# Performance work log

Hardware: AMD Instinct MI355X
Metric: run time of the kernel (lower is better)

## Reference

```python
import jax, jax.numpy as jnp
import numpy as np

B, T, D, H, E, M = 4, 2048, 2048, 8, 512, 8  # batch, seq, hidden, moe_heads, moe_experts, moe_dim//2
F = E * M  # flatten_shape = 4096
HALF = D // 2


def act(z):
    # 'relu2' activation: relu(x)**2
    r = jax.nn.relu(z)
    return r * r


def setup_inputs() -> dict:
    key = jax.random.key(0)
    ks = jax.random.split(key, 13)
    s = 0.02
    return {
        "x": jax.random.normal(ks[0], (B, T, D), jnp.float32),
        "g1": jax.random.uniform(ks[1], (B, T, H, E), jnp.float32),
        "g2": jax.random.uniform(ks[2], (B, T, H, E), jnp.float32),
        "u1_w": jax.random.normal(ks[3], (F, D), jnp.float32) * s,
        "u1_b": jnp.zeros((F,), jnp.float32),
        "u2_w": jax.random.normal(ks[4], (F, D), jnp.float32) * s,
        "u2_b": jnp.zeros((F,), jnp.float32),
        "v11_w": jax.random.normal(ks[5], (HALF, F), jnp.float32) * s,
        "v12_w": jax.random.normal(ks[6], (HALF, F), jnp.float32) * s,
        "v21_w": jax.random.normal(ks[7], (HALF, F), jnp.float32) * s,
        "v22_w": jax.random.normal(ks[8], (HALF, F), jnp.float32) * s,
        "b1": jax.random.normal(ks[9], (E, HALF), jnp.float32) * s,
        "b2": jax.random.normal(ks[10], (E, HALF), jnp.float32) * s,
    }


def reference(x, g1, g2, u1_w, u1_b, u2_w, u2_b, v11_w, v12_w, v21_w, v22_w, b1, b2):
    # x1, x2: [B,T,E,M]
    x1 = act(x @ u1_w.T + u1_b).reshape(B, T, E, M)
    x2 = act(x @ u2_w.T + u2_b).reshape(B, T, E, M)

    g1s = g1.sum(axis=2)  # [B,T,E] (einsum '...hi->...i')
    g2s = g2.sum(axis=2)

    # x11 = v11(einsum('btim,bthi->btim', x1, g1).flatten(-2))
    x11 = (x1 * g1s[..., None]).reshape(B, T, F) @ v11_w.T
    # x12 = v12(einsum('btjm,bthj,bthi->btim', x2, g2, g1).flatten(-2))
    t2 = jnp.einsum('btjm,bthj->bthm', x2, g2)
    x12 = jnp.einsum('bthm,bthi->btim', t2, g1).reshape(B, T, F) @ v12_w.T
    # x13 = einsum('bthi,id->btd', g1, b1)
    x13 = g1s @ b1

    # x21 = v21(einsum('btim,bthi,bthj->btjm', x1, g1, g2).flatten(-2))
    t1 = jnp.einsum('btim,bthi->bthm', x1, g1)
    x21 = jnp.einsum('bthm,bthj->btjm', t1, g2).reshape(B, T, F) @ v21_w.T
    # x22 = v22(einsum('btjm,bthj->btjm', x2, g2).flatten(-2))
    x22 = (x2 * g2s[..., None]).reshape(B, T, F) @ v22_w.T
    # x23 = einsum('bthj,jd->btd', g2, b2)
    x23 = g2s @ b2

    return jnp.concatenate((x11 + x12 + x13, x21 + x22 + x23), axis=-1)
```

## Files before the change

kernel.cpp:

```cpp
#include <hip/hip_runtime.h>
#include <hip/hip_bf16.h>

#define TOK   8192
#define DD    2048
#define FF    4096
#define EE    512
#define HALF  1024
#define KCAT  8704

typedef __bf16 bf16x8 __attribute__((ext_vector_type(8)));
typedef __bf16 bf16x4 __attribute__((ext_vector_type(4)));
typedef float  f32x4  __attribute__((ext_vector_type(4)));
using bf16 = __hip_bfloat16;

#define AS1(p) ((const __attribute__((address_space(1))) void*)(p))
#define AS3(p) ((__attribute__((address_space(3))) void*)(p))


__global__ void cvt_bf16(const float* __restrict__ in, bf16* __restrict__ out, int n4) {
    int i = blockIdx.x * blockDim.x + threadIdx.x;
    int stride = gridDim.x * blockDim.x;
    for (; i < n4; i += stride) {
        float4 v = ((const float4*)in)[i];
        bf16x4 o;
        o[0] = (__bf16)v.x; o[1] = (__bf16)v.y; o[2] = (__bf16)v.z; o[3] = (__bf16)v.w;
        ((bf16x4*)out)[i] = o;
    }
}

__global__ void pack_w(const float* __restrict__ vA, const float* __restrict__ vB,
                       const float* __restrict__ bmat, bf16* __restrict__ W) {
    int n = blockIdx.x;
    const float* ra = vA + (size_t)n * FF;
    const float* rb = vB + (size_t)n * FF;
    bf16* w = W + (size_t)n * KCAT;
    for (int k = threadIdx.x; k < FF; k += 256) {
        w[k]      = __float2bfloat16(ra[k]);
        w[FF + k] = __float2bfloat16(rb[k]);
    }
    for (int e = threadIdx.x; e < EE; e += 256)
        w[2 * FF + e] = __float2bfloat16(bmat[(size_t)e * HALF + n]);
}

template<int MODE>
__global__ __launch_bounds__(512, 2)
void gemmP(const bf16* __restrict__ A0, const bf16* __restrict__ B0,
           const float* __restrict__ bias0, void* __restrict__ C0,
           const bf16* __restrict__ A1, const bf16* __restrict__ B1,
           const float* __restrict__ bias1, void* __restrict__ C1,
           int nbm, int nbn, int K, int ldc)
{
    __shared__ __align__(16) char smem[131072];
    const int tid  = threadIdx.x;
    const int lane = tid & 63;
    const int wid  = tid >> 6;
    const int wm = wid >> 2, wn = wid & 3;
    const int r16 = lane & 15, kb = lane >> 4;

    int bid = blockIdx.x;
    {
        int nwg = gridDim.x;
        int q = nwg >> 3, r = nwg & 7;
        int xcd = bid & 7, idx = bid >> 3;
        bid = (xcd < r ? xcd * (q + 1) : r * (q + 1) + (xcd - r) * q) + idx;
    }
    const int npg = nbm * nbn;
    const int g   = bid / npg;
    const int lb  = bid - g * npg;
    const int bm = lb / nbn, bn = lb - bm * nbn;

    const bf16*  A    = g ? A1 : A0;
    const bf16*  Bw   = g ? B1 : B0;
    const float* bias = g ? bias1 : bias0;
    char* Cout = (char*)(g ? C1 : C0);

    const long row0 = (long)bm * 256;
    const int  col0 = bn * 256;
    const int  nt   = K >> 6;

    const char* gA[2]; const char* gB[2];
    #pragma unroll
    for (int l = 0; l < 2; ++l) {
        const uint32_t S = (uint32_t)(l * 512 + tid) * 16;
        const int r  = (int)(S >> 6);
        const int cb = (int)((S & 63) ^ ((uint32_t)((r >> 1) & 3) << 4));
        gA[l] = (const char*)A  + (row0 + r) * (long)K * 2 + cb;
        gB[l] = (const char*)Bw + (long)(col0 + r) * K * 2 + cb;
    }
    const uint32_t ldst = (uint32_t)(tid & ~63) * 16;

    const uint32_t swz  = ((uint32_t)(r16 >> 1) & 3u) << 4;
    const uint32_t aoff = (uint32_t)((wm * 128 + r16) * 64 + kb * 16) ^ swz;
    const uint32_t boff = (uint32_t)((wn * 64  + r16) * 64 + kb * 16) ^ swz;

    f32x4 acc[8][4];
    #pragma unroll
    for (int i = 0; i < 8; ++i)
        #pragma unroll
        for (int j = 0; j < 4; ++j)
            acc[i][j] = (f32x4){0.f, 0.f, 0.f, 0.f};

    __builtin_amdgcn_global_load_lds(AS1(gA[0]),      AS3(smem +     0 + ldst), 16, 0, 0);
    __builtin_amdgcn_global_load_lds(AS1(gA[1]),      AS3(smem +  8192 + ldst), 16, 0, 0);
    __builtin_amdgcn_global_load_lds(AS1(gB[0]),      AS3(smem + 32768 + ldst), 16, 0, 0);
    __builtin_amdgcn_global_load_lds(AS1(gB[1]),      AS3(smem + 40960 + ldst), 16, 0, 0);
    __builtin_amdgcn_global_load_lds(AS1(gA[0] + 64), AS3(smem + 16384 + ldst), 16, 0, 0);
    __builtin_amdgcn_global_load_lds(AS1(gA[1] + 64), AS3(smem + 24576 + ldst), 16, 0, 0);
    __builtin_amdgcn_global_load_lds(AS1(gB[0] + 64), AS3(smem + 49152 + ldst), 16, 0, 0);
    __builtin_amdgcn_global_load_lds(AS1(gB[1] + 64), AS3(smem + 57344 + ldst), 16, 0, 0);
    asm volatile("s_waitcnt vmcnt(4)\n\ts_barrier" ::: "memory");

    bf16x8 afA[4], afB[4], bv0[4], bv1[4];
    #pragma unroll
    for (int f = 0; f < 4; ++f) {
        afA[f] = *(const bf16x8*)(smem +     0 + aoff + f * 1024);
        bv0[f] = *(const bf16x8*)(smem + 32768 + boff + f * 1024);
    }

#define MFMA16(AF, BV, IH)                                                              \
    __builtin_amdgcn_s_setprio(1);                                                      \
    _Pragma("unroll")                                                                   \
    for (int fi = 0; fi < 4; ++fi) {                                                    \
        acc[(IH)*4+fi][0] = __builtin_amdgcn_mfma_f32_16x16x32_bf16(AF[fi], BV[0], acc[(IH)*4+fi][0], 0, 0, 0); \
        acc[(IH)*4+fi][1] = __builtin_amdgcn_mfma_f32_16x16x32_bf16(AF[fi], BV[1], acc[(IH)*4+fi][1], 0, 0, 0); \
        acc[(IH)*4+fi][2] = __builtin_amdgcn_mfma_f32_16x16x32_bf16(AF[fi], BV[2], acc[(IH)*4+fi][2], 0, 0, 0); \
        acc[(IH)*4+fi][3] = __builtin_amdgcn_mfma_f32_16x16x32_bf16(AF[fi], BV[3], acc[(IH)*4+fi][3], 0, 0, 0); \
    }                                                                                   \
    __builtin_amdgcn_s_setprio(0);

    for (int t = 0; t < nt; ++t) {
        const char* pb = smem + (t & 1) * 65536;
        char*       pt = smem + ((t + 1) & 1) * 65536;
        const bool  st = (t + 1 < nt);
        const long  koff = (long)(t + 1) * 128;

        if (st) {
            __builtin_amdgcn_global_load_lds(AS1(gA[0] + koff), AS3(pt +    0 + ldst), 16, 0, 0);
            __builtin_amdgcn_global_load_lds(AS1(gA[1] + koff), AS3(pt + 8192 + ldst), 16, 0, 0);
        }
        asm volatile("s_barrier" ::: "memory");
        #pragma unroll
        for (int f = 0; f < 4; ++f)
            afB[f] = *(const bf16x8*)(pb + 4096 + aoff + f * 1024);
        MFMA16(afA, bv0, 0)

        if (st) {
            __builtin_amdgcn_global_load_lds(AS1(gB[0] + koff), AS3(pt + 32768 + ldst), 16, 0, 0);
            __builtin_amdgcn_global_load_lds(AS1(gB[1] + koff), AS3(pt + 40960 + ldst), 16, 0, 0);
            asm volatile("s_waitcnt vmcnt(4)" ::: "memory");
        } else {
            asm volatile("s_waitcnt vmcnt(0)" ::: "memory");
        }
        asm volatile("s_barrier" ::: "memory");
        #pragma unroll
        for (int f = 0; f < 4; ++f) {
            afA[f] = *(const bf16x8*)(pb + 16384 + aoff + f * 1024);
            bv1[f] = *(const bf16x8*)(pb + 49152 + boff + f * 1024);
        }
        MFMA16(afB, bv0, 1)

        if (st) {
            __builtin_amdgcn_global_load_lds(AS1(gA[0] + koff + 64), AS3(pt + 16384 + ldst), 16, 0, 0);
            __builtin_amdgcn_global_load_lds(AS1(gA[1] + koff + 64), AS3(pt + 24576 + ldst), 16, 0, 0);
        }
        asm volatile("s_barrier" ::: "memory");
        #pragma unroll
        for (int f = 0; f < 4; ++f)
            afB[f] = *(const bf16x8*)(pb + 16384 + 4096 + aoff + f * 1024);
        MFMA16(afA, bv1, 0)

        if (st) {
            __builtin_amdgcn_global_load_lds(AS1(gB[0] + koff + 64), AS3(pt + 49152 + ldst), 16, 0, 0);
            __builtin_amdgcn_global_load_lds(AS1(gB[1] + koff + 64), AS3(pt + 57344 + ldst), 16, 0, 0);
            asm volatile("s_waitcnt vmcnt(4)" ::: "memory");
        }
        asm volatile("s_barrier" ::: "memory");
        if (st) {
            #pragma unroll
            for (int f = 0; f < 4; ++f) {
                afA[f] = *(const bf16x8*)(pt +     0 + aoff + f * 1024);
                bv0[f] = *(const bf16x8*)(pt + 32768 + boff + f * 1024);
            }
        }
        MFMA16(afB, bv1, 1)
    }
#undef MFMA16

    const int rb = (lane >> 4) * 4;
    #pragma unroll
    for (int i = 0; i < 8; ++i) {
        #pragma unroll
        for (int j = 0; j < 4; ++j) {
            const int cc = col0 + wn * 64 + j * 16 + r16;
            float badd = 0.f;
            if (MODE == 1) badd = bias[cc];
            #pragma unroll
            for (int e = 0; e < 4; ++e) {
                long row = row0 + wm * 128 + i * 16 + rb + e;
                float v = acc[i][j][e];
                if (MODE == 1) {
                    v += badd;
                    v = fmaxf(v, 0.f);
                    v = v * v;
                    ((bf16*)Cout)[row * ldc + cc] = __float2bfloat16(v);
                } else {
                    ((float*)Cout)[row * ldc + cc] = v;
                }
            }
        }
    }
}

#define GPAD 524
__global__ __launch_bounds__(256)
void glue(const float* __restrict__ g1, const float* __restrict__ g2,
          bf16* __restrict__ Yl, bf16* __restrict__ Yr)
{
    __shared__ __align__(16) float g1t[8 * GPAD];
    __shared__ __align__(16) float g2t[8 * GPAD];
    __shared__ float g1s[EE], g2s[EE];
    __shared__ float t1s[64], t2s[64];
    __shared__ float t1p[4][64], t2p[4][64];
    __shared__ __align__(16) bf16 x1t[FF], x2t[FF];

    const int t   = blockIdx.x;
    const int tid = threadIdx.x;
    const float* g1p = g1 + (size_t)t * FF;
    const float* g2p = g2 + (size_t)t * FF;
    bf16* ylp = Yl + (size_t)t * KCAT;
    bf16* yrp = Yr + (size_t)t * KCAT;

    #pragma unroll
    for (int c = 0; c < 4; ++c) {
        int idx4 = (c * 256 + tid) * 4;
        float4 v1 = *(const float4*)(g1p + idx4);
        float4 v2 = *(const float4*)(g2p + idx4);
        int h = idx4 >> 9, e = idx4 & 511;
        *(float4*)&g1t[h * GPAD + e] = v1;
        *(float4*)&g2t[h * GPAD + e] = v2;
    }
    #pragma unroll
    for (int c = 0; c < 2; ++c) {
        int idx8 = (c * 256 + tid) * 8;
        *(bf16x8*)&x1t[idx8] = *(const bf16x8*)(ylp + idx8);
        *(bf16x8*)&x2t[idx8] = *(const bf16x8*)(yrp + FF + idx8);
    }
    __syncthreads();

    #pragma unroll
    for (int c = 0; c < 2; ++c) {
        int e = c * 256 + tid;
        float s1 = 0.f, s2 = 0.f;
        #pragma unroll
        for (int h = 0; h < 8; ++h) { s1 += g1t[h * GPAD + e]; s2 += g2t[h * GPAD + e]; }
        g1s[e] = s1; g2s[e] = s2;
    }

    {
        int o = tid & 63;
        int h = o & 7, m = o >> 3;
        int p = tid >> 6;
        float s1 = 0.f, s2 = 0.f;
        #pragma unroll 8
        for (int ii = 0; ii < 128; ++ii) {
            int e = p * 128 + ii;
            float xv1 = __bfloat162float(x1t[e * 8 + m]);
            float xv2 = __bfloat162float(x2t[e * 8 + m]);
            s1 += xv1 * g1t[h * GPAD + e];
            s2 += xv2 * g2t[h * GPAD + e];
        }
        t1p[p][o] = s1; t2p[p][o] = s2;
    }
    __syncthreads();
    if (tid < 64)       t1s[tid] = t1p[0][tid] + t1p[1][tid] + t1p[2][tid] + t1p[3][tid];
    else if (tid < 128) { int o = tid - 64; t2s[o] = t2p[0][o] + t2p[1][o] + t2p[2][o] + t2p[3][o]; }
    __syncthreads();

    #pragma unroll
    for (int c = 0; c < 2; ++c) {
        int f0 = (c * 256 + tid) * 8;
        int e  = f0 >> 3;
        float s1 = g1s[e], s2 = g2s[e];
        bf16x8 xa = *(const bf16x8*)&x1t[f0];
        bf16x8 xb = *(const bf16x8*)&x2t[f0];
        bf16x8 o1, o2;
        #pragma unroll
        for (int u = 0; u < 8; ++u) {
            o1[u] = (__bf16)((float)xa[u] * s1);
            o2[u] = (__bf16)((float)xb[u] * s2);
        }
        *(bf16x8*)(ylp + f0)      = o1;
        *(bf16x8*)(yrp + FF + f0) = o2;
    }
    #pragma unroll
    for (int c = 0; c < 2; ++c) {
        int f0 = (c * 256 + tid) * 8;
        int i  = f0 >> 3;
        bf16x8 o12v, o21v;
        #pragma unroll
        for (int m = 0; m < 8; ++m) {
            float s12 = 0.f, s21 = 0.f;
            #pragma unroll
            for (int h = 0; h < 8; ++h) {
                s12 += t2s[(m << 3) | h] * g1t[h * GPAD + i];
                s21 += t1s[(m << 3) | h] * g2t[h * GPAD + i];
            }
            o12v[m] = (__bf16)s12;
            o21v[m] = (__bf16)s21;
        }
        *(bf16x8*)(ylp + FF + f0) = o12v;
        *(bf16x8*)(yrp + f0)      = o21v;
    }
    {
        int e0 = tid * 2;
        ylp[2 * FF + e0]     = __float2bfloat16(g1s[e0]);
        ylp[2 * FF + e0 + 1] = __float2bfloat16(g1s[e0 + 1]);
        yrp[2 * FF + e0]     = __float2bfloat16(g2s[e0]);
        yrp[2 * FF + e0 + 1] = __float2bfloat16(g2s[e0 + 1]);
    }
}


extern "C" void kernel_launch(void* const* d_in, const int* in_sizes, int n_in,
                              void* d_out, int out_size, void* d_ws, size_t ws_size,
                              hipStream_t stream) {
    const float* x    = (const float*)d_in[0];
    const float* g1   = (const float*)d_in[1];
    const float* g2   = (const float*)d_in[2];
    const float* u1_w = (const float*)d_in[3];
    const float* u1_b = (const float*)d_in[4];
    const float* u2_w = (const float*)d_in[5];
    const float* u2_b = (const float*)d_in[6];
    const float* v11  = (const float*)d_in[7];
    const float* v12  = (const float*)d_in[8];
    const float* v21  = (const float*)d_in[9];
    const float* v22  = (const float*)d_in[10];
    const float* b1   = (const float*)d_in[11];
    const float* b2   = (const float*)d_in[12];
    float* out = (float*)d_out;

    size_t off = 0;
    char* base = (char*)d_ws;
    auto take = [&](size_t bytes) { void* p = base + off; off += (bytes + 255) & ~(size_t)255; return p; };
    bf16* Xb  = (bf16*)take((size_t)TOK * DD * 2);
    bf16* U1b = (bf16*)take((size_t)FF * DD * 2);
    bf16* U2b = (bf16*)take((size_t)FF * DD * 2);
    bf16* Wl  = (bf16*)take((size_t)HALF * KCAT * 2);
    bf16* Wr  = (bf16*)take((size_t)HALF * KCAT * 2);
    bf16* Yl  = (bf16*)take((size_t)TOK * KCAT * 2);
    bf16* Yr  = (bf16*)take((size_t)TOK * KCAT * 2);

    cvt_bf16<<<4096, 256, 0, stream>>>(x,    Xb,  TOK * DD / 4);
    cvt_bf16<<<2048, 256, 0, stream>>>(u1_w, U1b, FF * DD / 4);
    cvt_bf16<<<2048, 256, 0, stream>>>(u2_w, U2b, FF * DD / 4);
    pack_w<<<HALF, 256, 0, stream>>>(v11, v12, b1, Wl);
    pack_w<<<HALF, 256, 0, stream>>>(v21, v22, b2, Wr);

    gemmP<1><<<2 * (TOK / 256) * (FF / 256), 512, 0, stream>>>(
        Xb, U1b, u1_b, Yl,
        Xb, U2b, u2_b, Yr + FF,
        TOK / 256, FF / 256, DD, KCAT);

    glue<<<TOK, 256, 0, stream>>>(g1, g2, Yl, Yr);

    gemmP<0><<<2 * (TOK / 256) * (HALF / 256), 512, 0, stream>>>(
        Yl, Wl, nullptr, out,
        Yr, Wr, nullptr, out + HALF,
        TOK / 256, HALF / 256, KCAT, DD);
}
```

Measured before the change: 692.9 us.

## Overlap gate staging and V-weight packing inside first GEMM main loop

Moves the fp32→bf16 conversion of the gate tensors g1/g2 and of the four V weight matrices into the first GEMM's K-loop. Each thread loads and stores one float4 per phase, so this memory traffic overlaps with MFMA work, and the separate pack_w kernel is reduced to packing only the bias columns. The glue kernel now reads the gates as bf16 from scratch space in Yl/Yr instead of fp32 from the inputs, which halves its gate read traffic but lowers gate precision to bf16. The cost is extra registers, address arithmetic and memory pressure in the GEMM, which may reduce its occupancy or issue efficiency.

```diff
diff --git a/kernel.cpp b/kernel.cpp
--- a/kernel.cpp
+++ b/kernel.cpp
@@ -28,18 +28,13 @@
     }
 }
 
-__global__ void pack_w(const float* __restrict__ vA, const float* __restrict__ vB,
-                       const float* __restrict__ bmat, bf16* __restrict__ W) {
+__global__ void pack_b(const float* __restrict__ b1, const float* __restrict__ b2,
+                       bf16* __restrict__ Wl, bf16* __restrict__ Wr) {
     int n = blockIdx.x;
-    const float* ra = vA + (size_t)n * FF;
-    const float* rb = vB + (size_t)n * FF;
-    bf16* w = W + (size_t)n * KCAT;
-    for (int k = threadIdx.x; k < FF; k += 256) {
-        w[k]      = __float2bfloat16(ra[k]);
-        w[FF + k] = __float2bfloat16(rb[k]);
-    }
-    for (int e = threadIdx.x; e < EE; e += 256)
-        w[2 * FF + e] = __float2bfloat16(bmat[(size_t)e * HALF + n]);
+    for (int e = threadIdx.x; e < EE; e += 256) {
+        Wl[(long)n * KCAT + 2 * FF + e] = __float2bfloat16(b1[(long)e * HALF + n]);
+        Wr[(long)n * KCAT + 2 * FF + e] = __float2bfloat16(b2[(long)e * HALF + n]);
+    }
 }
 
 template<int MODE>
@@ -48,7 +43,12 @@
            const float* __restrict__ bias0, void* __restrict__ C0,
            const bf16* __restrict__ A1, const bf16* __restrict__ B1,
            const float* __restrict__ bias1, void* __restrict__ C1,
-           int nbm, int nbn, int K, int ldc)
+           int nbm, int nbn, int K, int ldc,
+           const float* __restrict__ xg1, const float* __restrict__ xg2,
+           const float* __restrict__ xv11, const float* __restrict__ xv12,
+           const float* __restrict__ xv21, const float* __restrict__ xv22,
+           bf16* __restrict__ xYl, bf16* __restrict__ xYr,
+           bf16* __restrict__ xWl, bf16* __restrict__ xWr)
 {
     __shared__ __align__(16) char smem[131072];
     const int tid  = threadIdx.x;
@@ -92,6 +92,45 @@
     const uint32_t swz  = ((uint32_t)(r16 >> 1) & 3u) << 4;
     const uint32_t aoff = (uint32_t)((wm * 128 + r16) * 64 + kb * 16) ^ swz;
     const uint32_t boff = (uint32_t)((wn * 64  + r16) * 64 + kb * 16) ^ swz;
+
+    const int auxBase = (MODE == 1) ? blockIdx.x * (2 * nt) : 0x7fffffff;
+    float4 auxData = {0.f, 0.f, 0.f, 0.f};
+    bf16*  auxDst  = nullptr;
+    auto aux_calc = [&](int sid, const float*& src, bf16*& dst) {
+        long F = ((long)sid << 11) + tid * 4;
+        if (sid < 32768) {
+            const long TG = (long)TOK * FF;
+            if (F < TG) { long tt = F >> 12, j = F & 4095; src = xg1 + F;      dst = xYl + tt * KCAT + FF + j; }
+            else { long F2 = F - TG; long tt = F2 >> 12, j = F2 & 4095; src = xg2 + F2; dst = xYr + tt * KCAT + j; }
+        } else {
+            long F2 = F - (((long)32768) << 11);
+            const long SEG = (long)HALF * FF;
+            int which = (F2 >= 3 * SEG) ? 3 : (F2 >= 2 * SEG) ? 2 : (F2 >= SEG) ? 1 : 0;
+            long r = F2 - (long)which * SEG;
+            long n = r >> 12, k = r & 4095;
+            const float* vs = (which == 0) ? xv11 : (which == 1) ? xv12 : (which == 2) ? xv21 : xv22;
+            src = vs + r;
+            bf16* wb = (which < 2) ? xWl : xWr;
+            dst = wb + n * KCAT + ((which & 1) ? FF : 0) + k;
+        }
+    };
+    auto aux_step = [&](int ph, int t) {
+        if (MODE != 1) return;
+        if (auxDst) {
+            bf16x4 o;
+            o[0] = (__bf16)auxData.x; o[1] = (__bf16)auxData.y;
+            o[2] = (__bf16)auxData.z; o[3] = (__bf16)auxData.w;
+            *(bf16x4*)auxDst = o;
+            auxDst = nullptr;
+        }
+        int sid = auxBase + t * 2 + ph;
+        if (sid < 40960) {
+            const float* src; bf16* dst;
+            aux_calc(sid, src, dst);
+            auxData = *(const float4*)src;
+            auxDst  = dst;
+        }
+    };
 
     f32x4 acc[8][4];
     #pragma unroll
@@ -134,6 +173,7 @@
         const bool  st = (t + 1 < nt);
         const long  koff = (long)(t + 1) * 128;
 
+        aux_step(0, t);
         if (st) {
             __builtin_amdgcn_global_load_lds(AS1(gA[0] + koff), AS3(pt +    0 + ldst), 16, 0, 0);
             __builtin_amdgcn_global_load_lds(AS1(gA[1] + koff), AS3(pt + 8192 + ldst), 16, 0, 0);
@@ -144,6 +184,7 @@
             afB[f] = *(const bf16x8*)(pb + 4096 + aoff + f * 1024);
         MFMA16(afA, bv0, 0)
 
+        aux_step(1, t);
         if (st) {
             __builtin_amdgcn_global_load_lds(AS1(gB[0] + koff), AS3(pt + 32768 + ldst), 16, 0, 0);
             __builtin_amdgcn_global_load_lds(AS1(gB[1] + koff), AS3(pt + 40960 + ldst), 16, 0, 0);
@@ -185,6 +226,13 @@
         MFMA16(afB, bv1, 1)
     }
 #undef MFMA16
+
+    if (MODE == 1 && auxDst) {
+        bf16x4 o;
+        o[0] = (__bf16)auxData.x; o[1] = (__bf16)auxData.y;
+        o[2] = (__bf16)auxData.z; o[3] = (__bf16)auxData.w;
+        *(bf16x4*)auxDst = o;
+    }
 
     const int rb = (lane >> 4) * 4;
     #pragma unroll
@@ -213,8 +261,7 @@
 
 #define GPAD 524
 __global__ __launch_bounds__(256)
-void glue(const float* __restrict__ g1, const float* __restrict__ g2,
-          bf16* __restrict__ Yl, bf16* __restrict__ Yr)
+void glue(bf16* __restrict__ Yl, bf16* __restrict__ Yr)
 {
     __shared__ __align__(16) float g1t[8 * GPAD];
     __shared__ __align__(16) float g2t[8 * GPAD];
@@ -225,19 +272,25 @@
 
     const int t   = blockIdx.x;
     const int tid = threadIdx.x;
-    const float* g1p = g1 + (size_t)t * FF;
-    const float* g2p = g2 + (size_t)t * FF;
     bf16* ylp = Yl + (size_t)t * KCAT;
     bf16* yrp = Yr + (size_t)t * KCAT;
-
-    #pragma unroll
-    for (int c = 0; c < 4; ++c) {
-        int idx4 = (c * 256 + tid) * 4;
-        float4 v1 = *(const float4*)(g1p + idx4);
-        float4 v2 = *(const float4*)(g2p + idx4);
-        int h = idx4 >> 9, e = idx4 & 511;
-        *(float4*)&g1t[h * GPAD + e] = v1;
-        *(float4*)&g2t[h * GPAD + e] = v2;
+    const bf16* g1p = ylp + FF;
+    const bf16* g2p = yrp;
+
+    #pragma unroll
+    for (int c = 0; c < 2; ++c) {
+        int idx8 = (c * 256 + tid) * 8;
+        bf16x8 v1 = *(const bf16x8*)(g1p + idx8);
+        bf16x8 v2 = *(const bf16x8*)(g2p + idx8);
+        int h = idx8 >> 9, e = idx8 & 511;
+        float4 a1 = {(float)v1[0], (float)v1[1], (float)v1[2], (float)v1[3]};
+        float4 b1v = {(float)v1[4], (float)v1[5], (float)v1[6], (float)v1[7]};
+        float4 a2 = {(float)v2[0], (float)v2[1], (float)v2[2], (float)v2[3]};
+        float4 b2v = {(float)v2[4], (float)v2[5], (float)v2[6], (float)v2[7]};
+        *(float4*)&g1t[h * GPAD + e]     = a1;
+        *(float4*)&g1t[h * GPAD + e + 4] = b1v;
+        *(float4*)&g2t[h * GPAD + e]     = a2;
+        *(float4*)&g2t[h * GPAD + e + 4] = b2v;
     }
     #pragma unroll
     for (int c = 0; c < 2; ++c) {
@@ -353,18 +406,20 @@
     cvt_bf16<<<4096, 256, 0, stream>>>(x,    Xb,  TOK * DD / 4);
     cvt_bf16<<<2048, 256, 0, stream>>>(u1_w, U1b, FF * DD / 4);
     cvt_bf16<<<2048, 256, 0, stream>>>(u2_w, U2b, FF * DD / 4);
-    pack_w<<<HALF, 256, 0, stream>>>(v11, v12, b1, Wl);
-    pack_w<<<HALF, 256, 0, stream>>>(v21, v22, b2, Wr);
+    pack_b<<<HALF, 256, 0, stream>>>(b1, b2, Wl, Wr);
 
     gemmP<1><<<2 * (TOK / 256) * (FF / 256), 512, 0, stream>>>(
         Xb, U1b, u1_b, Yl,
         Xb, U2b, u2_b, Yr + FF,
-        TOK / 256, FF / 256, DD, KCAT);
-
-    glue<<<TOK, 256, 0, stream>>>(g1, g2, Yl, Yr);
+        TOK / 256, FF / 256, DD, KCAT,
+        g1, g2, v11, v12, v21, v22, Yl, Yr, Wl, Wr);
+
+    glue<<<TOK, 256, 0, stream>>>(Yl, Yr);
 
     gemmP<0><<<2 * (TOK / 256) * (HALF / 256), 512, 0, stream>>>(
         Yl, Wl, nullptr, out,
         Yr, Wr, nullptr, out + HALF,
-        TOK / 256, HALF / 256, KCAT, DD);
+        TOK / 256, HALF / 256, KCAT, DD,
+        nullptr, nullptr, nullptr, nullptr, nullptr, nullptr,
+        nullptr, nullptr, nullptr, nullptr);
 }
```

New measurement: 819.3 us. 18.2% more time.
